# Kernel tuning notes

Hardware: AMD Instinct MI355X
Metric: run time of the kernel (lower is better)

The kernel has to match this reference:

```python
import jax, jax.numpy as jnp
import numpy as np

D_MODEL = 1024
H = 16
D_K = D_MODEL // H
WINDOW = 256
NEG = -1.0e9


def setup_inputs() -> dict:
    key = jax.random.key(0)
    ks = jax.random.split(key, 12)
    B, S = 1, 4096
    scale = 1.0 / np.sqrt(D_MODEL)
    inp = {
        'q': jax.random.normal(ks[0], (B, S, D_MODEL), dtype=jnp.float32),
        'k': jax.random.normal(ks[1], (B, S, D_MODEL), dtype=jnp.float32),
        'v': jax.random.normal(ks[2], (B, S, D_MODEL), dtype=jnp.float32),
        'w_q': jax.random.normal(ks[3], (D_MODEL, D_MODEL), dtype=jnp.float32) * scale,
        'b_q': jnp.zeros((D_MODEL,), dtype=jnp.float32),
        'w_k': jax.random.normal(ks[4], (D_MODEL, D_MODEL), dtype=jnp.float32) * scale,
        'b_k': jnp.zeros((D_MODEL,), dtype=jnp.float32),
        'w_v': jax.random.normal(ks[5], (D_MODEL, D_MODEL), dtype=jnp.float32) * scale,
        'b_v': jnp.zeros((D_MODEL,), dtype=jnp.float32),
        'w_o': jax.random.normal(ks[6], (D_MODEL, D_MODEL), dtype=jnp.float32) * scale,
        'b_o': jnp.zeros((D_MODEL,), dtype=jnp.float32),
    }
    return inp


def _local_mask(seq_len: int, window_size: int) -> jnp.ndarray:
    left = (window_size - 1) // 2
    right = window_size - 1 - left
    row = jnp.arange(seq_len)[:, None]
    col = jnp.arange(seq_len)[None, :]
    return (col >= row - left) & (col <= row + right)  # [S, S] bool


def reference(q, k, v, w_q, b_q, w_k, b_k, w_v, b_v, w_o, b_o):
    B, Sq, _ = q.shape
    Sk = k.shape[1]
    # projections (torch Linear: x @ W.T + b) -> [B, h, S, d_k]
    query = (q @ w_q.T + b_q).reshape(B, Sq, H, D_K).transpose(0, 2, 1, 3)
    key = (k @ w_k.T + b_k).reshape(B, Sk, H, D_K).transpose(0, 2, 1, 3)
    value = (v @ w_v.T + b_v).reshape(B, Sk, H, D_K).transpose(0, 2, 1, 3)

    scores = jnp.einsum('bhqd,bhkd->bhqk', query, key) / jnp.sqrt(
        jnp.asarray(D_K, dtype=query.dtype))
    if Sq == Sk:
        mask = _local_mask(Sq, WINDOW)  # [S, S]
        scores = jnp.where(mask[None, None], scores, jnp.asarray(NEG, scores.dtype))
    attn = jax.nn.softmax(scores, axis=-1)
    x = jnp.einsum('bhqk,bhkd->bhqd', attn, value)
    x = x.transpose(0, 2, 1, 3).reshape(B, Sq, D_MODEL)
    return x @ w_o.T + b_o
```

## Files before the change

kernel.cpp:

```cpp
#include <hip/hip_runtime.h>

#define SEQ 4096
#define DM 1024
#define NH 16
#define DK 64
#define NT 10

typedef _Float16 half8 __attribute__((ext_vector_type(8)));
typedef _Float16 half4v __attribute__((ext_vector_type(4)));
typedef float f32x4 __attribute__((ext_vector_type(4)));

#define MFMA16(a, b, c) __builtin_amdgcn_mfma_f32_16x16x32_f16((a), (b), (c), 0, 0, 0)

__global__ void cvt_all(const float* __restrict__ q, const float* __restrict__ k,
                        const float* __restrict__ v, const float* __restrict__ wq,
                        const float* __restrict__ wk, const float* __restrict__ wv,
                        const float* __restrict__ wo, _Float16* __restrict__ qh,
                        _Float16* __restrict__ kh, _Float16* __restrict__ vh,
                        _Float16* __restrict__ wqh, _Float16* __restrict__ wkh,
                        _Float16* __restrict__ wvh, _Float16* __restrict__ woh) {
    int z = blockIdx.y;
    const float* src;
    _Float16* dst;
    int n;
    switch (z) {
    case 0: src = q;  dst = qh;  n = SEQ * DM; break;
    case 1: src = k;  dst = kh;  n = SEQ * DM; break;
    case 2: src = v;  dst = vh;  n = SEQ * DM; break;
    case 3: src = wq; dst = wqh; n = DM * DM;  break;
    case 4: src = wk; dst = wkh; n = DM * DM;  break;
    case 5: src = wv; dst = wvh; n = DM * DM;  break;
    default: src = wo; dst = woh; n = DM * DM; break;
    }
    int idx = (blockIdx.x * 256 + threadIdx.x) * 4;
    if (idx >= n) return;
    float4 f = *(const float4*)(src + idx);
    half4v h;
    h[0] = (_Float16)f.x; h[1] = (_Float16)f.y; h[2] = (_Float16)f.z; h[3] = (_Float16)f.w;
    *(half4v*)(dst + idx) = h;
}

template <int MT>
__device__ __forceinline__ void gemm_core(const _Float16* __restrict__ A,
                                          const _Float16* __restrict__ B,
                                          const float* __restrict__ bias,
                                          void* __restrict__ Cout, int mode, float scale) {
    const int K = DM;
    const int N = DM;
    constexpr int MI = MT / 32;
    constexpr int ACH = MT / 64;
    __shared__ _Float16 As[MT * 32];
    __shared__ _Float16 Bs[128 * 32];
    int tid = threadIdx.x;
    int wave = tid >> 6, lane = tid & 63;
    int quad = lane >> 4, l16 = lane & 15;
    int m0 = blockIdx.x * MT;
    int n0 = blockIdx.y * 128;
    int wr = (wave >> 1) * (MT / 2);
    int wc = (wave & 1) * 64;
    f32x4 acc[MI][4] = {};

    for (int k0 = 0; k0 < K; k0 += 32) {
#pragma unroll
        for (int j = 0; j < ACH; ++j) {
            int c = j * 256 + tid;
            int row = c >> 2, cc = c & 3;
            const _Float16* ga = A + (size_t)(m0 + row) * K + k0 + cc * 8;
            __builtin_amdgcn_global_load_lds(
                (const __attribute__((address_space(1))) void*)ga,
                (__attribute__((address_space(3))) void*)(As + j * 2048 + wave * 512), 16, 0, 0);
        }
#pragma unroll
        for (int j = 0; j < 2; ++j) {
            int c = j * 256 + tid;
            int row = c >> 2, cc = c & 3;
            const _Float16* gb = B + (size_t)(n0 + row) * K + k0 + cc * 8;
            __builtin_amdgcn_global_load_lds(
                (const __attribute__((address_space(1))) void*)gb,
                (__attribute__((address_space(3))) void*)(Bs + j * 2048 + wave * 512), 16, 0, 0);
        }
        __syncthreads();
        half8 af[MI], bf[4];
#pragma unroll
        for (int mi = 0; mi < MI; ++mi)
            af[mi] = *(const half8*)&As[(wr + mi * 16 + l16) * 32 + quad * 8];
#pragma unroll
        for (int ni = 0; ni < 4; ++ni)
            bf[ni] = *(const half8*)&Bs[(wc + ni * 16 + l16) * 32 + quad * 8];
#pragma unroll
        for (int mi = 0; mi < MI; ++mi)
#pragma unroll
            for (int ni = 0; ni < 4; ++ni)
                acc[mi][ni] = MFMA16(af[mi], bf[ni], acc[mi][ni]);
        __syncthreads();
    }

    float bs[4];
#pragma unroll
    for (int ni = 0; ni < 4; ++ni) bs[ni] = bias[n0 + wc + ni * 16 + l16];

    if (mode == 0) {
        _Float16* C = (_Float16*)Cout;
#pragma unroll
        for (int mi = 0; mi < MI; ++mi)
#pragma unroll
            for (int ni = 0; ni < 4; ++ni) {
                int m = m0 + wr + mi * 16 + quad * 4;
                int n = n0 + wc + ni * 16 + l16;
#pragma unroll
                for (int r = 0; r < 4; ++r)
                    C[(size_t)(m + r) * N + n] = (_Float16)((acc[mi][ni][r] + bs[ni]) * scale);
            }
    } else if (mode == 1) {
        _Float16* C = (_Float16*)Cout;
#pragma unroll
        for (int mi = 0; mi < MI; ++mi)
#pragma unroll
            for (int ni = 0; ni < 4; ++ni) {
                int m = m0 + wr + mi * 16 + quad * 4;
                int n = n0 + wc + ni * 16 + l16;
                half4v p;
#pragma unroll
                for (int r = 0; r < 4; ++r) p[r] = (_Float16)(acc[mi][ni][r] + bs[ni]);
                *(half4v*)(C + (size_t)n * SEQ + m) = p;
            }
    } else {
        float* C = (float*)Cout;
#pragma unroll
        for (int mi = 0; mi < MI; ++mi)
#pragma unroll
            for (int ni = 0; ni < 4; ++ni) {
                int m = m0 + wr + mi * 16 + quad * 4;
                int n = n0 + wc + ni * 16 + l16;
#pragma unroll
                for (int r = 0; r < 4; ++r)
                    C[(size_t)(m + r) * N + n] = acc[mi][ni][r] + bs[ni];
            }
    }
}

__global__ void gemm_qkv(const _Float16* __restrict__ qh, const _Float16* __restrict__ kh,
                         const _Float16* __restrict__ vh, const _Float16* __restrict__ wqh,
                         const _Float16* __restrict__ wkh, const _Float16* __restrict__ wvh,
                         const float* __restrict__ bq, const float* __restrict__ bk,
                         const float* __restrict__ bv, _Float16* __restrict__ Qo,
                         _Float16* __restrict__ Ko, _Float16* __restrict__ Vt) {
    int z = blockIdx.z;
    const _Float16 *A, *B;
    const float* bias;
    void* C;
    int mode;
    float scale;
    if (z == 0) { A = qh; B = wqh; bias = bq; C = Qo; mode = 0; scale = 0.125f; }
    else if (z == 1) { A = kh; B = wkh; bias = bk; C = Ko; mode = 0; scale = 1.0f; }
    else { A = vh; B = wvh; bias = bv; C = Vt; mode = 1; scale = 1.0f; }
    gemm_core<128>(A, B, bias, C, mode, scale);
}

__global__ void gemm_out(const _Float16* __restrict__ Xh, const _Float16* __restrict__ woh,
                         const float* __restrict__ bo, float* __restrict__ out) {
    gemm_core<64>(Xh, woh, bo, out, 2, 1.0f);
}

__global__ void __launch_bounds__(256, 3) attn_kernel(const _Float16* __restrict__ Q,
                                                      const _Float16* __restrict__ K,
                                                      const _Float16* __restrict__ Vt,
                                                      _Float16* __restrict__ X) {
    __shared__ _Float16 Pl[4][2][16][40];
    int tid = threadIdx.x;
    int wave = tid >> 6, lane = tid & 63;
    int quad = lane >> 4, l16 = lane & 15;
    int h = blockIdx.y;
    int q0 = blockIdx.x * 64 + wave * 16;

    const _Float16* Qp = Q + (size_t)(q0 + l16) * DM + h * DK + quad * 8;
    half8 aq0 = *(const half8*)(Qp);
    half8 aq1 = *(const half8*)(Qp + 32);

    int kstart = (q0 > 127) ? ((q0 - 127) & ~31) : 0;

    f32x4 s[NT][2];
#pragma unroll
    for (int t = 0; t < NT; ++t) {
        int kt = kstart + t * 32;
#pragma unroll
        for (int cf = 0; cf < 2; ++cf) {
            int krow = kt + cf * 16 + l16;
            int kc = krow < SEQ ? krow : SEQ - 1;
            const _Float16* Kp = K + (size_t)kc * DM + h * DK + quad * 8;
            half8 b0 = *(const half8*)(Kp);
            half8 b1 = *(const half8*)(Kp + 32);
            f32x4 z = {};
            z = MFMA16(aq0, b0, z);
            z = MFMA16(aq1, b1, z);
            s[t][cf] = z;
        }
    }

#pragma unroll
    for (int t = 0; t < NT; ++t)
#pragma unroll
        for (int cf = 0; cf < 2; ++cf) {
            int key = kstart + t * 32 + cf * 16 + l16;
#pragma unroll
            for (int r = 0; r < 4; ++r) {
                int row = q0 + quad * 4 + r;
                bool valid = (key >= row - 127) && (key <= row + 128) && (key < SEQ);
                if (!valid) s[t][cf][r] = -1e30f;
            }
        }
    float rowM[4];
#pragma unroll
    for (int r = 0; r < 4; ++r) {
        float m = -1e30f;
#pragma unroll
        for (int t = 0; t < NT; ++t) m = fmaxf(m, fmaxf(s[t][0][r], s[t][1][r]));
#pragma unroll
        for (int off = 1; off < 16; off <<= 1) m = fmaxf(m, __shfl_xor(m, off));
        rowM[r] = m;
    }

    f32x4 o[4] = {};
    float sum[4] = {0.f, 0.f, 0.f, 0.f};
#pragma unroll
    for (int t = 0; t < NT; ++t) {
        int vcol = kstart + t * 32 + quad * 8;
        int vc = vcol < SEQ ? vcol : 0;
#pragma unroll
        for (int r = 0; r < 4; ++r) {
            float p0 = __expf(s[t][0][r] - rowM[r]);
            float p1 = __expf(s[t][1][r] - rowM[r]);
            Pl[wave][t & 1][quad * 4 + r][l16] = (_Float16)p0;
            Pl[wave][t & 1][quad * 4 + r][l16 + 16] = (_Float16)p1;
            sum[r] += p0 + p1;
        }
        half8 ap = *(const half8*)&Pl[wave][t & 1][l16][quad * 8];
#pragma unroll
        for (int ni = 0; ni < 4; ++ni) {
            const _Float16* Vp = Vt + (size_t)(h * DK + ni * 16 + l16) * SEQ + vc;
            half8 bv = *(const half8*)(Vp);
            o[ni] = MFMA16(ap, bv, o[ni]);
        }
    }

    float rinv[4];
#pragma unroll
    for (int r = 0; r < 4; ++r) {
        float sm = sum[r];
#pragma unroll
        for (int off = 1; off < 16; off <<= 1) sm += __shfl_xor(sm, off);
        rinv[r] = 1.0f / sm;
    }
#pragma unroll
    for (int ni = 0; ni < 4; ++ni) {
        int n = h * DK + ni * 16 + l16;
#pragma unroll
        for (int r = 0; r < 4; ++r) {
            int m = q0 + quad * 4 + r;
            X[(size_t)m * DM + n] = (_Float16)(o[ni][r] * rinv[r]);
        }
    }
}

extern "C" void kernel_launch(void* const* d_in, const int* in_sizes, int n_in, void* d_out,
                              int out_size, void* d_ws, size_t ws_size, hipStream_t stream) {
    const float* q  = (const float*)d_in[0];
    const float* k  = (const float*)d_in[1];
    const float* v  = (const float*)d_in[2];
    const float* wq = (const float*)d_in[3];
    const float* bq = (const float*)d_in[4];
    const float* wk = (const float*)d_in[5];
    const float* bk = (const float*)d_in[6];
    const float* wv = (const float*)d_in[7];
    const float* bv = (const float*)d_in[8];
    const float* wo = (const float*)d_in[9];
    const float* bo = (const float*)d_in[10];

    const size_t SZ_T = (size_t)SEQ * DM * sizeof(_Float16);
    const size_t SZ_W = (size_t)DM * DM * sizeof(_Float16);
    char* p = (char*)d_ws;
    _Float16* qh  = (_Float16*)(p);
    _Float16* kh  = (_Float16*)(p + SZ_T);
    _Float16* vh  = (_Float16*)(p + 2 * SZ_T);
    _Float16* wqh = (_Float16*)(p + 3 * SZ_T);
    _Float16* wkh = (_Float16*)(p + 3 * SZ_T + SZ_W);
    _Float16* wvh = (_Float16*)(p + 3 * SZ_T + 2 * SZ_W);
    _Float16* woh = (_Float16*)(p + 3 * SZ_T + 3 * SZ_W);
    _Float16* Qo  = (_Float16*)(p + 3 * SZ_T + 4 * SZ_W);
    _Float16* Ko  = (_Float16*)(p + 4 * SZ_T + 4 * SZ_W);
    _Float16* Vt  = (_Float16*)(p + 5 * SZ_T + 4 * SZ_W);
    _Float16* Xh  = qh;

    cvt_all<<<dim3(4096, 7), 256, 0, stream>>>(q, k, v, wq, wk, wv, wo, qh, kh, vh, wqh, wkh,
                                               wvh, woh);
    gemm_qkv<<<dim3(32, 8, 3), 256, 0, stream>>>(qh, kh, vh, wqh, wkh, wvh, bq, bk, bv, Qo, Ko,
                                                 Vt);
    attn_kernel<<<dim3(SEQ / 64, NH), 256, 0, stream>>>(Qo, Ko, Vt, Xh);
    gemm_out<<<dim3(64, 8), 256, 0, stream>>>(Xh, woh, bo, (float*)d_out);
}
```

Measured before the change: 229.8 us.

## Split attention key range across waves with shared-memory softmax merge

The attention kernel now has each block handle 16 query rows instead of 64. The key window is split across the four waves, with each wave doing 3 key tiles. Per-wave max, sum and partial outputs go to shared memory and are combined with a rescaled log-sum-exp merge, and each wave then writes one 16-column slice. This cuts the serial MFMA/exp chain per wave and quadruples the grid for better occupancy and latency hiding. In exchange it covers 12 tiles per row instead of 10, adds two block barriers and a shared-memory merge, and lowers the launch-bounds occupancy hint.

After: 228.5 us. No clear change (-0.5%).

```diff
diff --git a/kernel.cpp b/kernel.cpp
--- a/kernel.cpp
+++ b/kernel.cpp
@@ -4,7 +4,7 @@
 #define DM 1024
 #define NH 16
 #define DK 64
-#define NT 10
+#define NTW 3
 
 typedef _Float16 half8 __attribute__((ext_vector_type(8)));
 typedef _Float16 half4v __attribute__((ext_vector_type(4)));
@@ -162,16 +162,20 @@
     gemm_core<64>(Xh, woh, bo, out, 2, 1.0f);
 }
 
-__global__ void __launch_bounds__(256, 3) attn_kernel(const _Float16* __restrict__ Q,
+__global__ void __launch_bounds__(256, 2) attn_kernel(const _Float16* __restrict__ Q,
                                                       const _Float16* __restrict__ K,
                                                       const _Float16* __restrict__ Vt,
                                                       _Float16* __restrict__ X) {
-    __shared__ _Float16 Pl[4][2][16][40];
+    __shared__ char smem[512 + 4 * 64 * 20 * 4];
+    _Float16(*Pl)[2][16][40] = (_Float16(*)[2][16][40])smem;
+    float2* MS = (float2*)smem;
+    float* Ob = (float*)(smem + 512);
+
     int tid = threadIdx.x;
     int wave = tid >> 6, lane = tid & 63;
     int quad = lane >> 4, l16 = lane & 15;
     int h = blockIdx.y;
-    int q0 = blockIdx.x * 64 + wave * 16;
+    int q0 = blockIdx.x * 16;
 
     const _Float16* Qp = Q + (size_t)(q0 + l16) * DM + h * DK + quad * 8;
     half8 aq0 = *(const half8*)(Qp);
@@ -179,10 +183,10 @@
 
     int kstart = (q0 > 127) ? ((q0 - 127) & ~31) : 0;
 
-    f32x4 s[NT][2];
-#pragma unroll
-    for (int t = 0; t < NT; ++t) {
-        int kt = kstart + t * 32;
+    f32x4 s[NTW][2];
+#pragma unroll
+    for (int j = 0; j < NTW; ++j) {
+        int kt = kstart + (wave + 4 * j) * 32;
 #pragma unroll
         for (int cf = 0; cf < 2; ++cf) {
             int krow = kt + cf * 16 + l16;
@@ -193,20 +197,20 @@
             f32x4 z = {};
             z = MFMA16(aq0, b0, z);
             z = MFMA16(aq1, b1, z);
-            s[t][cf] = z;
-        }
-    }
-
-#pragma unroll
-    for (int t = 0; t < NT; ++t)
+            s[j][cf] = z;
+        }
+    }
+
+#pragma unroll
+    for (int j = 0; j < NTW; ++j)
 #pragma unroll
         for (int cf = 0; cf < 2; ++cf) {
-            int key = kstart + t * 32 + cf * 16 + l16;
+            int key = kstart + (wave + 4 * j) * 32 + cf * 16 + l16;
 #pragma unroll
             for (int r = 0; r < 4; ++r) {
                 int row = q0 + quad * 4 + r;
                 bool valid = (key >= row - 127) && (key <= row + 128) && (key < SEQ);
-                if (!valid) s[t][cf][r] = -1e30f;
+                if (!valid) s[j][cf][r] = -1e30f;
             }
         }
     float rowM[4];
@@ -214,7 +218,7 @@
     for (int r = 0; r < 4; ++r) {
         float m = -1e30f;
 #pragma unroll
-        for (int t = 0; t < NT; ++t) m = fmaxf(m, fmaxf(s[t][0][r], s[t][1][r]));
+        for (int j = 0; j < NTW; ++j) m = fmaxf(m, fmaxf(s[j][0][r], s[j][1][r]));
 #pragma unroll
         for (int off = 1; off < 16; off <<= 1) m = fmaxf(m, __shfl_xor(m, off));
         rowM[r] = m;
@@ -223,18 +227,18 @@
     f32x4 o[4] = {};
     float sum[4] = {0.f, 0.f, 0.f, 0.f};
 #pragma unroll
-    for (int t = 0; t < NT; ++t) {
-        int vcol = kstart + t * 32 + quad * 8;
+    for (int j = 0; j < NTW; ++j) {
+        int vcol = kstart + (wave + 4 * j) * 32 + quad * 8;
         int vc = vcol < SEQ ? vcol : 0;
 #pragma unroll
         for (int r = 0; r < 4; ++r) {
-            float p0 = __expf(s[t][0][r] - rowM[r]);
-            float p1 = __expf(s[t][1][r] - rowM[r]);
-            Pl[wave][t & 1][quad * 4 + r][l16] = (_Float16)p0;
-            Pl[wave][t & 1][quad * 4 + r][l16 + 16] = (_Float16)p1;
+            float p0 = __expf(s[j][0][r] - rowM[r]);
+            float p1 = __expf(s[j][1][r] - rowM[r]);
+            Pl[wave][j & 1][quad * 4 + r][l16] = (_Float16)p0;
+            Pl[wave][j & 1][quad * 4 + r][l16 + 16] = (_Float16)p1;
             sum[r] += p0 + p1;
         }
-        half8 ap = *(const half8*)&Pl[wave][t & 1][l16][quad * 8];
+        half8 ap = *(const half8*)&Pl[wave][j & 1][l16][quad * 8];
 #pragma unroll
         for (int ni = 0; ni < 4; ++ni) {
             const _Float16* Vp = Vt + (size_t)(h * DK + ni * 16 + l16) * SEQ + vc;
@@ -242,23 +246,55 @@
             o[ni] = MFMA16(ap, bv, o[ni]);
         }
     }
-
-    float rinv[4];
 #pragma unroll
     for (int r = 0; r < 4; ++r) {
         float sm = sum[r];
 #pragma unroll
         for (int off = 1; off < 16; off <<= 1) sm += __shfl_xor(sm, off);
-        rinv[r] = 1.0f / sm;
-    }
-#pragma unroll
-    for (int ni = 0; ni < 4; ++ni) {
-        int n = h * DK + ni * 16 + l16;
-#pragma unroll
-        for (int r = 0; r < 4; ++r) {
-            int m = q0 + quad * 4 + r;
-            X[(size_t)m * DM + n] = (_Float16)(o[ni][r] * rinv[r]);
-        }
+        sum[r] = sm;
+    }
+
+    __syncthreads();
+    if (l16 == 0) {
+#pragma unroll
+        for (int r = 0; r < 4; ++r)
+            MS[wave * 16 + quad * 4 + r] = make_float2(rowM[r], sum[r]);
+    }
+#pragma unroll
+    for (int ni = 0; ni < 4; ++ni)
+        *(f32x4*)&Ob[(wave * 64 + lane) * 20 + ni * 4] = o[ni];
+    __syncthreads();
+
+    int niq = wave;
+    float f[4][4], rinv[4];
+#pragma unroll
+    for (int r = 0; r < 4; ++r) {
+        float2 msv[4];
+        float M = -1e30f;
+#pragma unroll
+        for (int w = 0; w < 4; ++w) {
+            msv[w] = MS[w * 16 + quad * 4 + r];
+            M = fmaxf(M, msv[w].x);
+        }
+        float S = 0.f;
+#pragma unroll
+        for (int w = 0; w < 4; ++w) {
+            f[w][r] = __expf(msv[w].x - M);
+            S += f[w][r] * msv[w].y;
+        }
+        rinv[r] = 1.0f / S;
+    }
+    f32x4 acc = {};
+#pragma unroll
+    for (int w = 0; w < 4; ++w) {
+        f32x4 ov = *(const f32x4*)&Ob[(w * 64 + lane) * 20 + niq * 4];
+#pragma unroll
+        for (int r = 0; r < 4; ++r) acc[r] += f[w][r] * ov[r];
+    }
+#pragma unroll
+    for (int r = 0; r < 4; ++r) {
+        int m = q0 + quad * 4 + r;
+        X[(size_t)m * DM + h * DK + niq * 16 + l16] = (_Float16)(acc[r] * rinv[r]);
     }
 }
 
@@ -295,6 +331,6 @@
                                                wvh, woh);
     gemm_qkv<<<dim3(32, 8, 3), 256, 0, stream>>>(qh, kh, vh, wqh, wkh, wvh, bq, bk, bv, Qo, Ko,
                                                  Vt);
-    attn_kernel<<<dim3(SEQ / 64, NH), 256, 0, stream>>>(Qo, Ko, Vt, Xh);
+    attn_kernel<<<dim3(SEQ / 16, NH), 256, 0, stream>>>(Qo, Ko, Vt, Xh);
     gemm_out<<<dim3(64, 8), 256, 0, stream>>>(Xh, woh, bo, (float*)d_out);
 }
```
